# Kernel tuning notes

Measured on AMD Instinct MI355X. Metric: run time of the kernel, lower is better.

Reference implementation:

```python
import jax, jax.numpy as jnp
import numpy as np

# Dimensions: d_model D, heads H, head dim DH (H*DH==D), resonator freqs NF, FFN rank R
B, T, D, H, DH, NF, R = 2, 1024, 1024, 16, 64, 256, 4096
EPS_LN = 1e-5
EPS_ATTN = 1e-6


def setup_inputs() -> dict:
    key = jax.random.key(0)
    ks = jax.random.split(key, 16)
    n = lambda i, shape, s=0.02: jax.random.normal(ks[i], shape, dtype=jnp.float32) * s
    return {
        "x": jax.random.normal(ks[0], (B, T, D), dtype=jnp.float32),
        # resonator input projections
        "W_amp": n(1, (D, NF)), "b_amp": jnp.zeros((NF,), jnp.float32),
        "W_phi": n(2, (D, NF)), "b_phi": jnp.zeros((NF,), jnp.float32),
        # resonator dynamics: per-frequency rotation, retention logit, firing threshold
        "omega": jax.random.uniform(ks[3], (NF,), dtype=jnp.float32, minval=0.0, maxval=float(np.pi)),
        "ret_logit": jnp.full((NF,), 2.0, jnp.float32),
        "theta": jnp.full((NF,), 0.5, jnp.float32),
        # feat_proj: 3*NF -> D
        "W_feat": n(4, (3 * NF, D)), "b_feat": jnp.zeros((D,), jnp.float32),
        # linear attention projections (BDH-GPU style, relu feature map, no out proj)
        "Wq": n(5, (D, H * DH)), "Wk": n(6, (D, H * DH)), "Wv": n(7, (D, H * DH)),
        # per-head layernorm affine
        "lnh_w": jnp.ones((H, DH), jnp.float32), "lnh_b": jnp.zeros((H, DH), jnp.float32),
        # ReLU low-rank FFN (positive_out=True)
        "W1": n(8, (D, R)), "b1": jnp.zeros((R,), jnp.float32),
        "W2": n(9, (R, D)), "b2": jnp.zeros((D,), jnp.float32),
        # final layernorm
        "ln_w": jnp.ones((D,), jnp.float32), "ln_b": jnp.zeros((D,), jnp.float32),
    }


def reference(x, W_amp, b_amp, W_phi, b_phi, omega, ret_logit, theta,
              W_feat, b_feat, Wq, Wk, Wv, lnh_w, lnh_b,
              W1, b1, W2, b2, ln_w, ln_b):
    Bb, Tt, Dd = x.shape
    # --- resonator input field: complex polar(amp, phi) ---
    amp = jax.nn.softplus(x @ W_amp + b_amp)                 # [B,T,NF]
    phi = jnp.float32(np.pi) * jnp.tanh(x @ W_phi + b_phi)   # [B,T,NF]
    u = jax.lax.complex(amp * jnp.cos(phi), amp * jnp.sin(phi))  # complex64 [B,T,NF]
    # --- sequential complex resonator recurrence (the kernel-headroom scan) ---
    decay = jax.nn.sigmoid(ret_logit)                         # [NF]
    a = jax.lax.complex(decay * jnp.cos(omega), decay * jnp.sin(omega))  # [NF] complex

    def step(X, u_t):
        pre = a * X + u_t                                     # [B,NF] complex
        g = jax.nn.sigmoid(jnp.abs(pre) - theta)              # threshold-map gate
        Xn = pre * g.astype(pre.dtype)
        return Xn, Xn

    X0 = jnp.zeros((Bb, u.shape[-1]), jnp.complex64)
    _, Xs = jax.lax.scan(step, X0, jnp.swapaxes(u, 0, 1))     # [T,B,NF]
    Xs = jnp.swapaxes(Xs, 0, 1)                               # [B,T,NF]
    feat = jnp.concatenate([Xs.real, Xs.imag, jnp.abs(Xs)], axis=-1)  # [B,T,3NF]
    h = jax.nn.relu(feat @ W_feat + b_feat)                   # pos(feat_proj(feat)) -> [B,T,D]
    # --- causal linear attention (relu feature map, cumulative KV state) ---
    q = jax.nn.relu(h @ Wq).reshape(Bb, Tt, H, DH)
    k = jax.nn.relu(h @ Wk).reshape(Bb, Tt, H, DH)
    v = (h @ Wv).reshape(Bb, Tt, H, DH)
    kv = jnp.cumsum(k[..., :, None] * v[..., None, :], axis=1)  # [B,T,H,DH,DH]
    ksum = jnp.cumsum(k, axis=1)                                 # [B,T,H,DH]
    num = jnp.einsum('bthd,bthde->bthe', q, kv)
    den = jnp.einsum('bthd,bthd->bth', q, ksum)[..., None] + EPS_ATTN
    y = num / den                                                # [B,T,H,DH]
    # --- per-head layernorm ---
    mean = y.mean(-1, keepdims=True)
    var = y.var(-1, keepdims=True)
    y = (y - mean) / jnp.sqrt(var + EPS_LN) * lnh_w + lnh_b
    y = y.reshape(Bb, Tt, H * DH)                                # [B,T,D]
    # --- ReLU low-rank FFN, positive_out ---
    y = jax.nn.relu(jax.nn.relu(y @ W1 + b1) @ W2 + b2)
    # --- residual + layernorm ---
    z = x + y
    mu = z.mean(-1, keepdims=True)
    vz = z.var(-1, keepdims=True)
    out = (z - mu) / jnp.sqrt(vz + EPS_LN) * ln_w + ln_b
    return out
```

## Files before the change

### kernel.cpp

```cpp
#include <hip/hip_runtime.h>
#include <hip/hip_bf16.h>
#include <math.h>

#ifndef M_PI_F
#define M_PI_F 3.14159265358979323846f
#endif

static constexpr int Bb = 2, Tt = 1024, Dd = 1024, Hh = 16, DHh = 64, NFf = 256, Rr = 4096;
static constexpr int Mm = Bb * Tt;
static constexpr int CHK = 64, NCHK = Tt / CHK;
static constexpr int QS = 3072;

enum Epi { EPI_NONE = 0, EPI_RELU, EPI_QKV };

typedef __attribute__((ext_vector_type(8))) short bf16x8;
typedef __attribute__((ext_vector_type(4))) float f32x4;

__device__ inline float bf2f(unsigned short u) {
  union { unsigned int i; float f; } c;
  c.i = (unsigned int)u << 16;
  return c.f;
}

__device__ inline void gload16(const short* g, short* l) {
  __builtin_amdgcn_global_load_lds(
      (const __attribute__((address_space(1))) unsigned int*)g,
      (__attribute__((address_space(3))) unsigned int*)l, 16, 0, 0);
}

#define GSTAGE(bufsel, kk0)                                           \
  _Pragma("unroll") for (int si = 0; si < 4; ++si) {                  \
    const int s = wid + si * 4;                                       \
    gload16(A + (size_t)(m0 + s * 8 + srow) * ldk + (kk0) + skk,      \
            &lA[(bufsel) * 8192 + s * 512]);                          \
    gload16(BT + (size_t)(n0 + s * 8 + srow) * ldk + (kk0) + skk,     \
            &lB[(bufsel) * 8192 + s * 512]);                          \
  }

template <int EPI, int OUTBF, int SPLITK>
__global__ __launch_bounds__(256) void gemm_mfma(const short* __restrict__ A,
                                                 const short* __restrict__ BT,
                                                 const float* __restrict__ bias,
                                                 float* __restrict__ Cf,
                                                 __hip_bfloat16* __restrict__ Cb,
                                                 int M, int N, int ldk) {
  __shared__ short lA[2 * 128 * 64];
  __shared__ short lB[2 * 128 * 64];
  const int tid = threadIdx.x;
  const int wid = tid >> 6, lane = tid & 63;

  const int nwg = gridDim.x * gridDim.y;
  const int wg = blockIdx.y * gridDim.x + blockIdx.x;
  const int qq = nwg >> 3, rr = nwg & 7;
  const int xcd = wg & 7, idx = wg >> 3;
  const int wg2 = (xcd < rr ? xcd * (qq + 1) : rr * (qq + 1) + (xcd - rr) * qq) + idx;
  const int bx = wg2 % gridDim.x, by = wg2 / gridDim.x;

  const int m0 = by * 128, n0 = bx * 128;
  const int wm = (wid >> 1) * 64, wn = (wid & 1) * 64;
  const int srow = lane >> 3;
  const int skk = (((lane & 7) ^ (lane >> 3)) << 3);

  int kstart = 0, klen = ldk;
  if (SPLITK > 1) {
    klen = ldk / SPLITK;
    kstart = blockIdx.z * klen;
    if (OUTBF)
      Cb += (size_t)blockIdx.z * M * N;
    else
      Cf += (size_t)blockIdx.z * M * N;
  }
  const int kend = kstart + klen;

  f32x4 acc[4][4] = {};

  GSTAGE(0, kstart);
  int cur = 0;
  for (int k0 = kstart; k0 < kend; k0 += 64) {
    if (k0 + 64 < kend) {
      GSTAGE(cur ^ 1, k0 + 64);
      asm volatile("s_waitcnt vmcnt(8)" ::: "memory");
    } else {
      asm volatile("s_waitcnt vmcnt(0)" ::: "memory");
    }
    asm volatile("s_barrier" ::: "memory");
    const short* bA = &lA[cur * 8192];
    const short* bB = &lB[cur * 8192];
#pragma unroll
    for (int kk = 0; kk < 2; ++kk) {
      const int krd = kk * 32 + (lane >> 4) * 8;
      const int rsel = lane & 15;
      const int kswz = krd ^ ((rsel & 7) << 3);
      bf16x8 af[4], bfr[4];
#pragma unroll
      for (int i = 0; i < 4; ++i) {
        af[i] = *(const bf16x8*)&bA[(wm + i * 16 + rsel) * 64 + kswz];
        bfr[i] = *(const bf16x8*)&bB[(wn + i * 16 + rsel) * 64 + kswz];
      }
#pragma unroll
      for (int i = 0; i < 4; ++i)
#pragma unroll
        for (int j = 0; j < 4; ++j)
          acc[i][j] = __builtin_amdgcn_mfma_f32_16x16x32_bf16(af[i], bfr[j], acc[i][j], 0, 0, 0);
    }
    asm volatile("s_barrier" ::: "memory");
    cur ^= 1;
  }

  const int crow = (lane >> 4) * 4;
  const int ccol = lane & 15;
#pragma unroll
  for (int j = 0; j < 4; ++j) {
    const int col = n0 + wn + j * 16 + ccol;
    const float bv = bias ? bias[col] : 0.f;
#pragma unroll
    for (int i = 0; i < 4; ++i) {
#pragma unroll
      for (int r = 0; r < 4; ++r) {
        float v = acc[i][j][r] + bv;
        const int row = m0 + wm + i * 16 + crow + r;
        if (EPI == EPI_QKV) {
          const float vv = (col < 2048) ? fmaxf(v, 0.f) : v;
          Cb[(size_t)row * QS + col] = __float2bfloat16(vv);
        } else {
          if (EPI == EPI_RELU) v = fmaxf(v, 0.f);
          const size_t off = (size_t)row * N + col;
          if (OUTBF)
            Cb[off] = __float2bfloat16(v);
          else
            Cf[off] = v;
        }
      }
    }
  }
}

__device__ __forceinline__ void tc_tile(float (*tile)[33], const float* __restrict__ W,
                                        __hip_bfloat16* __restrict__ WT, int K, int N,
                                        int tlocal) {
  const int tilesN = N / 32;
  const int bk = (tlocal / tilesN) * 32, bn = (tlocal % tilesN) * 32;
  const int tx = threadIdx.x & 31, ty = threadIdx.x >> 5;
#pragma unroll
  for (int r = 0; r < 32; r += 8) tile[ty + r][tx] = W[(size_t)(bk + ty + r) * N + bn + tx];
  __syncthreads();
#pragma unroll
  for (int r = 0; r < 32; r += 8)
    WT[(size_t)(bn + ty + r) * K + bk + tx] = __float2bfloat16(tile[tx][ty + r]);
}

__global__ __launch_bounds__(256) void tc_first(const float* __restrict__ W_amp,
                                                const float* __restrict__ W_phi,
                                                __hip_bfloat16* __restrict__ WTamp,
                                                __hip_bfloat16* __restrict__ WTphi,
                                                const float* __restrict__ x,
                                                __hip_bfloat16* __restrict__ xb) {
  __shared__ float tile[32][33];
  const int bid = blockIdx.x;
  if (bid >= 512) {
    const int i = ((bid - 512) * 256 + threadIdx.x) * 4;
    const float4 v = *(const float4*)&x[i];
    xb[i + 0] = __float2bfloat16(v.x);
    xb[i + 1] = __float2bfloat16(v.y);
    xb[i + 2] = __float2bfloat16(v.z);
    xb[i + 3] = __float2bfloat16(v.w);
    return;
  }
  if (bid < 256)
    tc_tile(tile, W_amp, WTamp, 1024, 256, bid);
  else
    tc_tile(tile, W_phi, WTphi, 1024, 256, bid - 256);
}

__global__ __launch_bounds__(256) void reduce_polar(const __hip_bfloat16* __restrict__ part,
                                                    const float* __restrict__ b_amp,
                                                    const float* __restrict__ b_phi,
                                                    __hip_bfloat16* __restrict__ outr,
                                                    __hip_bfloat16* __restrict__ outi) {
  const int idx = blockIdx.x * 256 + threadIdx.x;
  const int row = idx >> 8, c = idx & 255;
  const size_t MN = (size_t)Mm * 512;
  const size_t pa = (size_t)row * 512 + c;
  const unsigned short* pu = (const unsigned short*)part;
  float a = bf2f(pu[pa]) + bf2f(pu[pa + MN]) + bf2f(pu[pa + 2 * MN]) + bf2f(pu[pa + 3 * MN]) +
            b_amp[c];
  float ph = bf2f(pu[pa + 256]) + bf2f(pu[pa + 256 + MN]) + bf2f(pu[pa + 256 + 2 * MN]) +
             bf2f(pu[pa + 256 + 3 * MN]) + b_phi[c];
  a = (a > 0.f) ? (a + log1pf(expf(-a))) : log1pf(expf(a));
  ph = M_PI_F * tanhf(ph);
  float s, co;
  sincosf(ph, &s, &co);
  outr[idx] = __float2bfloat16(a * co);
  outi[idx] = __float2bfloat16(a * s);
}

static constexpr int RES_P = 16;
static constexpr int RES_TC = 128;
static constexpr int RES_W = 128;

#define RES_LOAD(buf_r, buf_i, tg)                                        \
  if ((tg) < cend) {                                                      \
    _Pragma("unroll") for (int i = 0; i < RES_P; ++i) {                   \
      buf_r[i] = __bfloat162float(ur[bbase + (size_t)((tg) + i) * NFf]);  \
      buf_i[i] = __bfloat162float(ui[bbase + (size_t)((tg) + i) * NFf]);  \
    }                                                                     \
  }

#define RES_STEP(buf_r, buf_i, tg)                                      \
  {                                                                      \
    const bool wr_ = (tg) >= cstart;                                     \
    _Pragma("unroll") for (int i = 0; i < RES_P; ++i) {                  \
      const float pr = fmaf(ar, Xr, fmaf(-ai, Xi, buf_r[i]));            \
      const float pim = fmaf(ar, Xi, fmaf(ai, Xr, buf_i[i]));            \
      const float mag = __builtin_amdgcn_sqrtf(fmaf(pr, pr, pim * pim)); \
      const float g = __builtin_amdgcn_rcpf(1.f + __expf(th - mag));     \
      Xr = pr * g;                                                       \
      Xi = pim * g;                                                      \
      if (wr_) {                                                         \
        const size_t fb = ((size_t)b * Tt + (tg) + i) * (3 * NFf);       \
        featb[fb + f] = __float2bfloat16(Xr);                            \
        featb[fb + NFf + f] = __float2bfloat16(Xi);                      \
        featb[fb + 2 * NFf + f] = __float2bfloat16(mag * g);             \
      }                                                                  \
    }                                                                    \
  }

struct STDesc {
  const float* src[6];
  __hip_bfloat16* dst[6];
  const __hip_bfloat16* ur;
  const __hip_bfloat16* ui;
  const float* omega;
  const float* ret_logit;
  const float* theta;
  __hip_bfloat16* featb;
};

__global__ __launch_bounds__(256) void scan_and_tc(STDesc d) {
  __shared__ float tile[32][33];
  const int bid = blockIdx.x;
  if (bid < 64) {
    if (threadIdx.x >= 64) return;
    const int tc = bid & 7;
    const int fs = (bid >> 3) & 3;
    const int b = bid >> 5;
    const int f = fs * 64 + threadIdx.x;
    const int cstart = tc * RES_TC;
    const int cend = cstart + RES_TC;
    const int tbeg = (cstart >= RES_W) ? cstart - RES_W : 0;
    const __hip_bfloat16* ur = d.ur;
    const __hip_bfloat16* ui = d.ui;
    __hip_bfloat16* featb = d.featb;
    const float dec = 1.f / (1.f + __expf(-d.ret_logit[f]));
    float so, co;
    sincosf(d.omega[f], &so, &co);
    const float ar = dec * co, ai = dec * so;
    const float th = d.theta[f];
    const size_t bbase = (size_t)b * Tt * NFf + f;
    float Xr = 0.f, Xi = 0.f;
    float Ar[RES_P], Ai[RES_P], Br[RES_P], Bi[RES_P];
    RES_LOAD(Ar, Ai, tbeg);
    for (int t0 = tbeg; t0 < cend; t0 += 2 * RES_P) {
      RES_LOAD(Br, Bi, t0 + RES_P);
      RES_STEP(Ar, Ai, t0);
      RES_LOAD(Ar, Ai, t0 + 2 * RES_P);
      RES_STEP(Br, Bi, t0 + RES_P);
    }
    return;
  }
  constexpr int KS[6] = {768, 1024, 1024, 1024, 1024, 4096};
  constexpr int NS[6] = {1024, 1024, 1024, 1024, 4096, 1024};
  constexpr int CUM[7] = {0, 768, 1792, 2816, 3840, 7936, 12032};
  const int t = bid - 64;
  int w = 0;
#pragma unroll
  for (int i = 0; i < 6; ++i)
    if (t >= CUM[i + 1]) w = i + 1;
  tc_tile(tile, d.src[w], d.dst[w], KS[w], NS[w], t - CUM[w]);
}

__global__ __launch_bounds__(256) void attn_chunk_kv(const __hip_bfloat16* __restrict__ k,
                                                     const __hip_bfloat16* __restrict__ v,
                                                     float* __restrict__ S,
                                                     float* __restrict__ Ksum) {
  __shared__ float Ks[64][68], Vs[64][68];
  const int g = blockIdx.x;
  const int j = g & (NCHK - 1), bh = g >> 4;
  const int b = bh >> 4, h = bh & (Hh - 1);
  const int tid = threadIdx.x;
  const size_t rowbase = (size_t)(b * Tt + j * CHK) * QS + h * DHh;
  const unsigned short* ku = (const unsigned short*)k;
  const unsigned short* vu = (const unsigned short*)v;
  for (int l = tid; l < 4096; l += 256) {
    const int s = l >> 6, d = l & 63;
    Ks[s][d] = bf2f(ku[rowbase + (size_t)s * QS + d]);
    Vs[s][d] = bf2f(vu[rowbase + (size_t)s * QS + d]);
  }
  __syncthreads();
  const int d0 = tid & 63, eb = tid >> 6, e0 = eb * 16;
  float4 acc4[4] = {};
  float ks = 0.f;
  for (int s = 0; s < 64; ++s) {
    const float kd = Ks[s][d0];
    ks += kd;
#pragma unroll
    for (int i = 0; i < 4; ++i) {
      const float4 v4 = *(const float4*)&Vs[s][e0 + 4 * i];
      acc4[i].x = fmaf(kd, v4.x, acc4[i].x);
      acc4[i].y = fmaf(kd, v4.y, acc4[i].y);
      acc4[i].z = fmaf(kd, v4.z, acc4[i].z);
      acc4[i].w = fmaf(kd, v4.w, acc4[i].w);
    }
  }
  float* Sg = S + (size_t)g * 4096 + (size_t)d0 * 64 + e0;
#pragma unroll
  for (int i = 0; i < 4; ++i) *(float4*)&Sg[4 * i] = acc4[i];
  if (eb == 0) Ksum[(size_t)g * 64 + d0] = ks;
}

__global__ __launch_bounds__(256) void attn_prefix(float* __restrict__ S,
                                                   float* __restrict__ Ksum) {
  const int bid = blockIdx.x;
  const int tid = threadIdx.x;
  if (bid < 512) {
    const int bh = bid >> 4, r = bid & 15;
    const int de = r * 256 + tid;
    const size_t base = (size_t)bh * (NCHK * 4096) + de;
    float vv[NCHK];
#pragma unroll
    for (int j = 0; j < NCHK; ++j) vv[j] = S[base + (size_t)j * 4096];
    float run = 0.f;
#pragma unroll
    for (int j = 0; j < NCHK; ++j) {
      const float tmp = vv[j];
      S[base + (size_t)j * 4096] = run;
      run += tmp;
    }
  } else {
    const int cid = (bid - 512) * 256 + tid;
    const int bh = cid >> 6, d = cid & 63;
    const size_t base = (size_t)bh * (NCHK * 64) + d;
    float vv[NCHK];
#pragma unroll
    for (int j = 0; j < NCHK; ++j) vv[j] = Ksum[base + (size_t)j * 64];
    float run = 0.f;
#pragma unroll
    for (int j = 0; j < NCHK; ++j) {
      const float tmp = vv[j];
      Ksum[base + (size_t)j * 64] = run;
      run += tmp;
    }
  }
}

__global__ __launch_bounds__(256) void attn_out(const __hip_bfloat16* __restrict__ q,
                                                const __hip_bfloat16* __restrict__ k,
                                                const __hip_bfloat16* __restrict__ v,
                                                const float* __restrict__ S,
                                                const float* __restrict__ Ksum,
                                                const float* __restrict__ lnw,
                                                const float* __restrict__ lnb,
                                                __hip_bfloat16* __restrict__ yhb) {
  __shared__ float Qs[64][68];
  __shared__ float KVP[64][68];
  __shared__ float At[64][65];
  const int g = blockIdx.x;
  const int j = g & (NCHK - 1), bh = g >> 4;
  const int b = bh >> 4, h = bh & (Hh - 1);
  const int tid = threadIdx.x;
  const size_t rowbase = (size_t)(b * Tt + j * CHK) * QS + h * DHh;
  const unsigned short* qu = (const unsigned short*)q;
  const unsigned short* ku = (const unsigned short*)k;
  const unsigned short* vu = (const unsigned short*)v;
#define KSWZ(s, d) ((((d) >> 2) ^ (((s) >> 4) & 3)) * 4 + ((d) & 3))
  for (int l = tid; l < 4096; l += 256) {
    const int s = l >> 6, d = l & 63;
    Qs[s][d] = bf2f(qu[rowbase + (size_t)s * QS + d]);
    KVP[s][KSWZ(s, d)] = bf2f(ku[rowbase + (size_t)s * QS + d]);
  }
  __syncthreads();
  const int t = tid >> 2, sg = tid & 3;
  const float* pk = Ksum + (size_t)g * 64;
  float adot[16] = {};
  float qpk = 0.f;
  for (int c = 0; c < 16; ++c) {
    const float4 q4 = *(const float4*)&Qs[t][4 * c];
    const float4 pk4 = *(const float4*)&pk[4 * c];
    qpk = fmaf(q4.x, pk4.x, fmaf(q4.y, pk4.y, fmaf(q4.z, pk4.z, fmaf(q4.w, pk4.w, qpk))));
#pragma unroll
    for (int i = 0; i < 16; ++i) {
      const float4 k4 = *(const float4*)&KVP[sg * 16 + i][4 * (c ^ sg)];
      adot[i] = fmaf(q4.x, k4.x, fmaf(q4.y, k4.y, fmaf(q4.z, k4.z, fmaf(q4.w, k4.w, adot[i]))));
    }
  }
  float rs = 0.f;
#pragma unroll
  for (int i = 0; i < 16; ++i) {
    if (sg * 16 + i > t) adot[i] = 0.f;
    rs += adot[i];
  }
  rs += __shfl_xor(rs, 1);
  rs += __shfl_xor(rs, 2);
  const float den = qpk + rs + 1e-6f;
  __syncthreads();
#pragma unroll
  for (int i = 0; i < 16; ++i) At[sg * 16 + i][t] = adot[i];
  for (int l = tid; l < 4096; l += 256) {
    const int s = l >> 6, d = l & 63;
    KVP[s][KSWZ(s, d)] = bf2f(vu[rowbase + (size_t)s * QS + d]);
  }
  __syncthreads();
  const int e0 = sg * 16;
  float4 num[4] = {};
  for (int s = 0; s <= t; ++s) {
    const float av = At[s][t];
    const int x = (s >> 4) & 3;
#pragma unroll
    for (int i = 0; i < 4; ++i) {
      const float4 v4 = *(const float4*)&KVP[s][e0 + 4 * (i ^ x)];
      num[i].x = fmaf(av, v4.x, num[i].x);
      num[i].y = fmaf(av, v4.y, num[i].y);
      num[i].z = fmaf(av, v4.z, num[i].z);
      num[i].w = fmaf(av, v4.w, num[i].w);
    }
  }
  __syncthreads();
  const float* Pg = S + (size_t)g * 4096;
  for (int l = tid; l < 4096; l += 256) KVP[l >> 6][KSWZ(l >> 6, l & 63)] = Pg[l];
  __syncthreads();
  for (int d = 0; d < 64; ++d) {
    const float qd = Qs[t][d];
    const int x = (d >> 4) & 3;
#pragma unroll
    for (int i = 0; i < 4; ++i) {
      const float4 p4 = *(const float4*)&KVP[d][e0 + 4 * (i ^ x)];
      num[i].x = fmaf(qd, p4.x, num[i].x);
      num[i].y = fmaf(qd, p4.y, num[i].y);
      num[i].z = fmaf(qd, p4.z, num[i].z);
      num[i].w = fmaf(qd, p4.w, num[i].w);
    }
  }
#undef KSWZ
  const float inv = 1.f / den;
  float o[16];
#pragma unroll
  for (int i = 0; i < 4; ++i) {
    o[4 * i + 0] = num[i].x * inv;
    o[4 * i + 1] = num[i].y * inv;
    o[4 * i + 2] = num[i].z * inv;
    o[4 * i + 3] = num[i].w * inv;
  }
  float s1 = 0.f, s2 = 0.f;
#pragma unroll
  for (int i = 0; i < 16; ++i) {
    s1 += o[i];
    s2 += o[i] * o[i];
  }
  s1 += __shfl_xor(s1, 1);
  s1 += __shfl_xor(s1, 2);
  s2 += __shfl_xor(s2, 1);
  s2 += __shfl_xor(s2, 2);
  const float mean = s1 * (1.f / 64.f);
  const float var = s2 * (1.f / 64.f) - mean * mean;
  const float rsv = rsqrtf(var + 1e-5f);
  const float* wv = lnw + h * DHh + e0;
  const float* bv = lnb + h * DHh + e0;
  unsigned short ob[16];
#pragma unroll
  for (int i = 0; i < 16; ++i) {
    const float r = (o[i] - mean) * rsv * wv[i] + bv[i];
    __hip_bfloat16 hv = __float2bfloat16(r);
    ob[i] = *(unsigned short*)&hv;
  }
  unsigned short* yg =
      (unsigned short*)yhb + (size_t)(b * Tt + j * CHK + t) * Dd + h * DHh + e0;
#pragma unroll
  for (int i = 0; i < 4; ++i) *(ushort4*)&yg[4 * i] = *(ushort4*)&ob[4 * i];
}

__global__ __launch_bounds__(256) void final_ln(const float* __restrict__ x,
                                                const __hip_bfloat16* __restrict__ part,
                                                const float* __restrict__ b2,
                                                const float* __restrict__ w,
                                                const float* __restrict__ bb,
                                                float* __restrict__ out) {
  __shared__ float r1[4], r2[4];
  const int row = blockIdx.x;
  const int tid = threadIdx.x;
  const size_t off = (size_t)row * Dd + tid * 4;
  const size_t MN = (size_t)Mm * Dd;
  float acc4[4] = {0.f, 0.f, 0.f, 0.f};
#pragma unroll
  for (int z = 0; z < 4; ++z) {
    const ushort4 u = *(const ushort4*)&part[off + (size_t)z * MN];
    acc4[0] += bf2f(u.x);
    acc4[1] += bf2f(u.y);
    acc4[2] += bf2f(u.z);
    acc4[3] += bf2f(u.w);
  }
  const float4 bv = *(const float4*)&b2[tid * 4];
  const float4 xa = *(const float4*)&x[off];
  float z[4];
  z[0] = xa.x + fmaxf(acc4[0] + bv.x, 0.f);
  z[1] = xa.y + fmaxf(acc4[1] + bv.y, 0.f);
  z[2] = xa.z + fmaxf(acc4[2] + bv.z, 0.f);
  z[3] = xa.w + fmaxf(acc4[3] + bv.w, 0.f);
  float s1 = z[0] + z[1] + z[2] + z[3];
  float s2 = z[0] * z[0] + z[1] * z[1] + z[2] * z[2] + z[3] * z[3];
#pragma unroll
  for (int o = 1; o < 64; o <<= 1) {
    s1 += __shfl_xor(s1, o);
    s2 += __shfl_xor(s2, o);
  }
  const int wid = tid >> 6;
  if ((tid & 63) == 0) {
    r1[wid] = s1;
    r2[wid] = s2;
  }
  __syncthreads();
  const float t1 = r1[0] + r1[1] + r1[2] + r1[3];
  const float t2 = r2[0] + r2[1] + r2[2] + r2[3];
  const float mu = t1 * (1.f / Dd);
  const float var = t2 * (1.f / Dd) - mu * mu;
  const float rsv = rsqrtf(var + 1e-5f);
  float4 o4;
  float* op = &o4.x;
#pragma unroll
  for (int jj = 0; jj < 4; ++jj) op[jj] = (z[jj] - mu) * rsv * w[tid * 4 + jj] + bb[tid * 4 + jj];
  *(float4*)&out[off] = o4;
}

extern "C" void kernel_launch(void* const* d_in, const int* in_sizes, int n_in,
                              void* d_out, int out_size, void* d_ws, size_t ws_size,
                              hipStream_t stream) {
  const float* x = (const float*)d_in[0];
  const float* W_amp = (const float*)d_in[1];
  const float* b_amp = (const float*)d_in[2];
  const float* W_phi = (const float*)d_in[3];
  const float* b_phi = (const float*)d_in[4];
  const float* omega = (const float*)d_in[5];
  const float* ret_logit = (const float*)d_in[6];
  const float* theta = (const float*)d_in[7];
  const float* W_feat = (const float*)d_in[8];
  const float* b_feat = (const float*)d_in[9];
  const float* Wq = (const float*)d_in[10];
  const float* Wk = (const float*)d_in[11];
  const float* Wv = (const float*)d_in[12];
  const float* lnh_w = (const float*)d_in[13];
  const float* lnh_b = (const float*)d_in[14];
  const float* W1 = (const float*)d_in[15];
  const float* b1 = (const float*)d_in[16];
  const float* W2 = (const float*)d_in[17];
  const float* b2 = (const float*)d_in[18];
  const float* ln_w = (const float*)d_in[19];
  const float* ln_b = (const float*)d_in[20];

  char* p = (char*)d_ws;
  auto alloc = [&](size_t bytes) {
    char* r = p;
    p += (bytes + 255) & ~(size_t)255;
    return r;
  };
  __hip_bfloat16* xb = (__hip_bfloat16*)alloc((size_t)Mm * Dd * 2);
  __hip_bfloat16* urh = (__hip_bfloat16*)alloc((size_t)Mm * NFf * 2);
  __hip_bfloat16* uih = (__hip_bfloat16*)alloc((size_t)Mm * NFf * 2);
  __hip_bfloat16* WTamp = (__hip_bfloat16*)alloc((size_t)NFf * Dd * 2);
  __hip_bfloat16* WTphi = (__hip_bfloat16*)alloc((size_t)NFf * Dd * 2);
  __hip_bfloat16* WTfeat = (__hip_bfloat16*)alloc((size_t)Dd * 3 * NFf * 2);
  __hip_bfloat16* WTq = (__hip_bfloat16*)alloc((size_t)Dd * Dd * 2);
  __hip_bfloat16* WTk = (__hip_bfloat16*)alloc((size_t)Dd * Dd * 2);
  __hip_bfloat16* WTv = (__hip_bfloat16*)alloc((size_t)Dd * Dd * 2);
  __hip_bfloat16* WT1 = (__hip_bfloat16*)alloc((size_t)Rr * Dd * 2);
  __hip_bfloat16* WT2 = (__hip_bfloat16*)alloc((size_t)Dd * Rr * 2);
  __hip_bfloat16* hb = (__hip_bfloat16*)alloc((size_t)Mm * Dd * 2);
  __hip_bfloat16* qkvb = (__hip_bfloat16*)alloc((size_t)Mm * QS * 2);
  __hip_bfloat16* yhb = (__hip_bfloat16*)alloc((size_t)Mm * Dd * 2);
  float* S = (float*)alloc((size_t)Bb * Hh * NCHK * 4096 * 4);
  float* Ksum = (float*)alloc((size_t)Bb * Hh * NCHK * 64 * 4);
  __hip_bfloat16* f1b = (__hip_bfloat16*)alloc((size_t)Mm * Rr * 2);
  __hip_bfloat16* pamp = (__hip_bfloat16*)alloc((size_t)4 * Mm * 512 * 2);
  __hip_bfloat16* pffn2 = (__hip_bfloat16*)alloc((size_t)4 * Mm * Dd * 2);

  __hip_bfloat16* featb = xb;
  const __hip_bfloat16* q = qkvb;
  const __hip_bfloat16* k = qkvb + 1024;
  const __hip_bfloat16* v = qkvb + 2048;
  float* out = (float*)d_out;

  const dim3 blk(256);

  tc_first<<<dim3(2560), blk, 0, stream>>>(W_amp, W_phi, WTamp, WTphi, x, xb);

  gemm_mfma<EPI_NONE, 1, 4><<<dim3(512 / 128, Mm / 128, 4), blk, 0, stream>>>(
      (const short*)xb, (const short*)WTamp, nullptr, nullptr, pamp, Mm, 512, Dd);
  reduce_polar<<<dim3(Mm * NFf / 256), blk, 0, stream>>>(pamp, b_amp, b_phi, urh, uih);

  STDesc st;
  st.src[0] = W_feat; st.dst[0] = WTfeat;
  st.src[1] = Wq; st.dst[1] = WTq;
  st.src[2] = Wk; st.dst[2] = WTk;
  st.src[3] = Wv; st.dst[3] = WTv;
  st.src[4] = W1; st.dst[4] = WT1;
  st.src[5] = W2; st.dst[5] = WT2;
  st.ur = urh; st.ui = uih;
  st.omega = omega; st.ret_logit = ret_logit; st.theta = theta;
  st.featb = featb;
  scan_and_tc<<<dim3(64 + 12032), blk, 0, stream>>>(st);

  gemm_mfma<EPI_RELU, 1, 0><<<dim3(Dd / 128, Mm / 128), blk, 0, stream>>>(
      (const short*)featb, (const short*)WTfeat, b_feat, nullptr, hb, Mm, Dd, 3 * NFf);

  gemm_mfma<EPI_QKV, 1, 0><<<dim3(QS / 128, Mm / 128), blk, 0, stream>>>(
      (const short*)hb, (const short*)WTq, nullptr, nullptr, qkvb, Mm, QS, Dd);

  attn_chunk_kv<<<dim3(Bb * Hh * NCHK), blk, 0, stream>>>(k, v, S, Ksum);
  attn_prefix<<<dim3(520), blk, 0, stream>>>(S, Ksum);
  attn_out<<<dim3(Bb * Hh * NCHK), blk, 0, stream>>>(q, k, v, S, Ksum, lnh_w, lnh_b, yhb);

  gemm_mfma<EPI_RELU, 1, 0><<<dim3(Rr / 128, Mm / 128), blk, 0, stream>>>(
      (const short*)yhb, (const short*)WT1, b1, nullptr, f1b, Mm, Rr, Dd);

  gemm_mfma<EPI_NONE, 1, 4><<<dim3(Dd / 128, Mm / 128, 4), blk, 0, stream>>>(
      (const short*)f1b, (const short*)WT2, nullptr, nullptr, pffn2, Mm, Dd, Rr);

  final_ln<<<dim3(Mm), blk, 0, stream>>>(x, pffn2, b2, ln_w, ln_b, out);
}
```

Measured before the change: 174.4 us.

## Compute intra-chunk QK scores with MFMA and store KV chunk states in bf16

The intra-chunk Q·K^T scores in attn_out are now computed with bf16 MFMA instructions straight from global memory. The causal mask and per-row denominator partial sums are written to shared memory, and V is loaded in the same pass as Q, which removes a barrier and a second load phase. The per-chunk KV state S is stored and prefix-summed in bf16 instead of fp32, halving its memory traffic. In exchange, the running prefix sums are rounded to bf16 on every step, which reduces accuracy.

```diff
diff --git a/kernel.cpp b/kernel.cpp
--- a/kernel.cpp
+++ b/kernel.cpp
@@ -281,7 +281,7 @@
 
 __global__ __launch_bounds__(256) void attn_chunk_kv(const __hip_bfloat16* __restrict__ k,
                                                      const __hip_bfloat16* __restrict__ v,
-                                                     float* __restrict__ S,
+                                                     __hip_bfloat16* __restrict__ S,
                                                      float* __restrict__ Ksum) {
   __shared__ float Ks[64][68], Vs[64][68];
   const int g = blockIdx.x;
@@ -312,28 +312,41 @@
       acc4[i].w = fmaf(kd, v4.w, acc4[i].w);
     }
   }
-  float* Sg = S + (size_t)g * 4096 + (size_t)d0 * 64 + e0;
-#pragma unroll
-  for (int i = 0; i < 4; ++i) *(float4*)&Sg[4 * i] = acc4[i];
+  unsigned short* Sg = (unsigned short*)S + (size_t)g * 4096 + (size_t)d0 * 64 + e0;
+#pragma unroll
+  for (int i = 0; i < 4; ++i) {
+    ushort4 o;
+    __hip_bfloat16 h0 = __float2bfloat16(acc4[i].x);
+    __hip_bfloat16 h1 = __float2bfloat16(acc4[i].y);
+    __hip_bfloat16 h2 = __float2bfloat16(acc4[i].z);
+    __hip_bfloat16 h3 = __float2bfloat16(acc4[i].w);
+    o.x = *(unsigned short*)&h0;
+    o.y = *(unsigned short*)&h1;
+    o.z = *(unsigned short*)&h2;
+    o.w = *(unsigned short*)&h3;
+    *(ushort4*)&Sg[4 * i] = o;
+  }
   if (eb == 0) Ksum[(size_t)g * 64 + d0] = ks;
 }
 
-__global__ __launch_bounds__(256) void attn_prefix(float* __restrict__ S,
+__global__ __launch_bounds__(256) void attn_prefix(__hip_bfloat16* __restrict__ S,
                                                    float* __restrict__ Ksum) {
   const int bid = blockIdx.x;
   const int tid = threadIdx.x;
   if (bid < 512) {
     const int bh = bid >> 4, r = bid & 15;
     const int de = r * 256 + tid;
+    unsigned short* Su = (unsigned short*)S;
     const size_t base = (size_t)bh * (NCHK * 4096) + de;
     float vv[NCHK];
 #pragma unroll
-    for (int j = 0; j < NCHK; ++j) vv[j] = S[base + (size_t)j * 4096];
+    for (int j = 0; j < NCHK; ++j) vv[j] = bf2f(Su[base + (size_t)j * 4096]);
     float run = 0.f;
 #pragma unroll
     for (int j = 0; j < NCHK; ++j) {
       const float tmp = vv[j];
-      S[base + (size_t)j * 4096] = run;
+      __hip_bfloat16 hv = __float2bfloat16(run);
+      Su[base + (size_t)j * 4096] = *(unsigned short*)&hv;
       run += tmp;
     }
   } else {
@@ -356,14 +369,15 @@
 __global__ __launch_bounds__(256) void attn_out(const __hip_bfloat16* __restrict__ q,
                                                 const __hip_bfloat16* __restrict__ k,
                                                 const __hip_bfloat16* __restrict__ v,
-                                                const float* __restrict__ S,
+                                                const __hip_bfloat16* __restrict__ S,
                                                 const float* __restrict__ Ksum,
                                                 const float* __restrict__ lnw,
                                                 const float* __restrict__ lnb,
                                                 __hip_bfloat16* __restrict__ yhb) {
   __shared__ float Qs[64][68];
   __shared__ float KVP[64][68];
-  __shared__ float At[64][65];
+  __shared__ float At[64][66];
+  __shared__ float denp[4][64];
   const int g = blockIdx.x;
   const int j = g & (NCHK - 1), bh = g >> 4;
   const int b = bh >> 4, h = bh & (Hh - 1);
@@ -376,40 +390,51 @@
   for (int l = tid; l < 4096; l += 256) {
     const int s = l >> 6, d = l & 63;
     Qs[s][d] = bf2f(qu[rowbase + (size_t)s * QS + d]);
-    KVP[s][KSWZ(s, d)] = bf2f(ku[rowbase + (size_t)s * QS + d]);
+    KVP[s][KSWZ(s, d)] = bf2f(vu[rowbase + (size_t)s * QS + d]);
+  }
+  {
+    const int w4 = tid >> 6, ln = tid & 63;
+    const int fr = ln & 15;
+    const int kh = ln >> 4;
+    const unsigned short* kr = ku + rowbase + (size_t)(w4 * 16 + fr) * QS + kh * 8;
+    const bf16x8 a0 = *(const bf16x8*)&kr[0];
+    const bf16x8 a1 = *(const bf16x8*)&kr[32];
+    f32x4 accQK[4] = {};
+#pragma unroll
+    for (int tt = 0; tt < 4; ++tt) {
+      const unsigned short* qr = qu + rowbase + (size_t)(tt * 16 + fr) * QS + kh * 8;
+      const bf16x8 b0 = *(const bf16x8*)&qr[0];
+      const bf16x8 b1 = *(const bf16x8*)&qr[32];
+      accQK[tt] = __builtin_amdgcn_mfma_f32_16x16x32_bf16(a0, b0, accQK[tt], 0, 0, 0);
+      accQK[tt] = __builtin_amdgcn_mfma_f32_16x16x32_bf16(a1, b1, accQK[tt], 0, 0, 0);
+    }
+#pragma unroll
+    for (int tt = 0; tt < 4; ++tt) {
+      const int t = tt * 16 + fr;
+      float dp = 0.f;
+#pragma unroll
+      for (int r = 0; r < 4; ++r) {
+        const int s = w4 * 16 + kh * 4 + r;
+        const float val = (s <= t) ? accQK[tt][r] : 0.f;
+        At[s][t] = val;
+        dp += val;
+      }
+      dp += __shfl_xor(dp, 16);
+      dp += __shfl_xor(dp, 32);
+      if (ln < 16) denp[w4][t] = dp;
+    }
   }
   __syncthreads();
   const int t = tid >> 2, sg = tid & 3;
   const float* pk = Ksum + (size_t)g * 64;
-  float adot[16] = {};
   float qpk = 0.f;
+#pragma unroll
   for (int c = 0; c < 16; ++c) {
     const float4 q4 = *(const float4*)&Qs[t][4 * c];
     const float4 pk4 = *(const float4*)&pk[4 * c];
     qpk = fmaf(q4.x, pk4.x, fmaf(q4.y, pk4.y, fmaf(q4.z, pk4.z, fmaf(q4.w, pk4.w, qpk))));
-#pragma unroll
-    for (int i = 0; i < 16; ++i) {
-      const float4 k4 = *(const float4*)&KVP[sg * 16 + i][4 * (c ^ sg)];
-      adot[i] = fmaf(q4.x, k4.x, fmaf(q4.y, k4.y, fmaf(q4.z, k4.z, fmaf(q4.w, k4.w, adot[i]))));
-    }
-  }
-  float rs = 0.f;
-#pragma unroll
-  for (int i = 0; i < 16; ++i) {
-    if (sg * 16 + i > t) adot[i] = 0.f;
-    rs += adot[i];
-  }
-  rs += __shfl_xor(rs, 1);
-  rs += __shfl_xor(rs, 2);
-  const float den = qpk + rs + 1e-6f;
-  __syncthreads();
-#pragma unroll
-  for (int i = 0; i < 16; ++i) At[sg * 16 + i][t] = adot[i];
-  for (int l = tid; l < 4096; l += 256) {
-    const int s = l >> 6, d = l & 63;
-    KVP[s][KSWZ(s, d)] = bf2f(vu[rowbase + (size_t)s * QS + d]);
-  }
-  __syncthreads();
+  }
+  const float den = denp[0][t] + denp[1][t] + denp[2][t] + denp[3][t] + qpk + 1e-6f;
   const int e0 = sg * 16;
   float4 num[4] = {};
   for (int s = 0; s <= t; ++s) {
@@ -425,8 +450,8 @@
     }
   }
   __syncthreads();
-  const float* Pg = S + (size_t)g * 4096;
-  for (int l = tid; l < 4096; l += 256) KVP[l >> 6][KSWZ(l >> 6, l & 63)] = Pg[l];
+  const unsigned short* Pg = (const unsigned short*)S + (size_t)g * 4096;
+  for (int l = tid; l < 4096; l += 256) KVP[l >> 6][KSWZ(l >> 6, l & 63)] = bf2f(Pg[l]);
   __syncthreads();
   for (int d = 0; d < 64; ++d) {
     const float qd = Qs[t][d];
@@ -575,7 +600,7 @@
   __hip_bfloat16* hb = (__hip_bfloat16*)alloc((size_t)Mm * Dd * 2);
   __hip_bfloat16* qkvb = (__hip_bfloat16*)alloc((size_t)Mm * QS * 2);
   __hip_bfloat16* yhb = (__hip_bfloat16*)alloc((size_t)Mm * Dd * 2);
-  float* S = (float*)alloc((size_t)Bb * Hh * NCHK * 4096 * 4);
+  __hip_bfloat16* S = (__hip_bfloat16*)alloc((size_t)Bb * Hh * NCHK * 4096 * 2);
   float* Ksum = (float*)alloc((size_t)Bb * Hh * NCHK * 64 * 4);
   __hip_bfloat16* f1b = (__hip_bfloat16*)alloc((size_t)Mm * Rr * 2);
   __hip_bfloat16* pamp = (__hip_bfloat16*)alloc((size_t)4 * Mm * 512 * 2);
```

After: 171.4 us. No clear change (-1.7%).
